# Performance work log

Hardware: AMD Instinct MI355X
Metric: run time of the kernel (lower is better)

Reference implementation:

```python
import jax, jax.numpy as jnp
import numpy as np

B, IN, HS, NM = 256, 512, 512, 1

def setup_inputs() -> dict:
    key = jax.random.key(0)
    ks = jax.random.split(key, 12)
    def kaiming(k, shape):
        fan_in = shape[0]
        bound = float(np.sqrt(6.0 / fan_in))  # kaiming_uniform with a=sqrt(5) approx; use gain sqrt(2): bound = sqrt(6/fan_in)
        return jax.random.uniform(k, shape, jnp.float32, -bound, bound)
    return {
        "x_t":  jax.random.normal(ks[0], (B, IN), jnp.float32),
        "h_t":  jax.random.normal(ks[1], (B, HS), jnp.float32),
        "c_t":  jax.random.normal(ks[2], (B, HS), jnp.float32),
        "hebb": jax.random.normal(ks[3], (B, HS, HS), jnp.float32) * 0.1,
        "W":    kaiming(ks[4], (IN, 4 * HS)),
        "U":    kaiming(ks[5], (HS, 4 * HS)),
        "bias": jnp.zeros((4 * HS,), jnp.float32),
        "alpha": jax.random.normal(ks[6], (1, 1, HS), jnp.float32) * 1e-4,
        "nm_w": jax.random.normal(ks[7], (NM, HS), jnp.float32),
        "nm_b": jnp.zeros((NM,), jnp.float32),
        "mt_w": jax.random.normal(ks[8], (HS, NM), jnp.float32),
        "mt_b": jnp.zeros((HS,), jnp.float32),
    }

def reference(x_t, h_t, c_t, hebb, W, U, bias, alpha, nm_w, nm_b, mt_w, mt_b):
    # g_t_hebb = h_t (B,1,HS) @ (alpha*hebb) (B,HS,HS) -> (B,HS)
    g_t_hebb = jnp.einsum('bh,bhk->bk', h_t, alpha * hebb)
    gates = x_t @ W + h_t @ U + bias                        # (B, 4*HS)
    i_t = jax.nn.sigmoid(gates[:, :HS])
    f_t = jax.nn.sigmoid(gates[:, HS:2 * HS])
    g_t = jnp.tanh(gates[:, 2 * HS:3 * HS] + g_t_hebb)
    o_t = jax.nn.sigmoid(gates[:, 3 * HS:])
    # rank-1 outer product per batch element: (B,HS,1)@(B,1,HS)
    delta_hebb = jnp.einsum('bi,bj->bij', h_t, g_t)         # (B,HS,HS)
    m_t = jnp.tanh(h_t @ nm_w.T + nm_b)                     # (B,NM)
    m_t = m_t @ mt_w.T + mt_b                               # (B,HS)
    hebb_new = jnp.clip(hebb + m_t[:, None, :] * delta_hebb, -2.0, 2.0)
    c_new = f_t * c_t + i_t * g_t
    h_new = o_t * jnp.tanh(c_new)
    return h_new, c_new, hebb_new
```

## Files before the change

kernel.cpp:

```cpp
#include <hip/hip_runtime.h>
#include <math.h>


#define HSZ 512
#define G4  2048

__device__ __forceinline__ float sigm(float x) { return 1.0f / (1.0f + __expf(-x)); }
__device__ __forceinline__ float clip2(float v) { return fminf(fmaxf(v, -2.0f), 2.0f); }

__global__ __launch_bounds__(256, 4)
void gates_gemm(const float* __restrict__ x, const float* __restrict__ h,
                const float* __restrict__ W, const float* __restrict__ U,
                const float* __restrict__ bias, float* __restrict__ gates)
{
    __shared__ float As[16][68];
    __shared__ float Bs[16][64];

    const int t     = threadIdx.x;
    const int brow0 = blockIdx.y * 64;
    const int bcol0 = blockIdx.x * 64;

    const int tr = t & 15;
    const int tc = t >> 4;
    const int arow = t >> 2, ak4 = (t & 3) * 4;
    const int brow = t >> 4, bc4 = (t & 15) * 4;

    float acc[4][4] = {};

    for (int ks = 0; ks < 64; ++ks) {
        const float* srcA;
        const float* srcB;
        int k0;
        if (ks < 32) { srcA = x; srcB = W; k0 = ks * 16; }
        else         { srcA = h; srcB = U; k0 = ks * 16 - 512; }

        float4 av = *(const float4*)&srcA[(size_t)(brow0 + arow) * 512 + k0 + ak4];
        float4 bv = *(const float4*)&srcB[(size_t)(k0 + brow) * 2048 + bcol0 + bc4];

        __syncthreads();
        As[ak4 + 0][arow] = av.x;
        As[ak4 + 1][arow] = av.y;
        As[ak4 + 2][arow] = av.z;
        As[ak4 + 3][arow] = av.w;
        *(float4*)&Bs[brow][bc4] = bv;
        __syncthreads();

        #pragma unroll
        for (int kk = 0; kk < 16; ++kk) {
            float4 a = *(float4*)&As[kk][tr * 4];
            float4 b = *(float4*)&Bs[kk][tc * 4];
            acc[0][0] += a.x * b.x; acc[0][1] += a.x * b.y; acc[0][2] += a.x * b.z; acc[0][3] += a.x * b.w;
            acc[1][0] += a.y * b.x; acc[1][1] += a.y * b.y; acc[1][2] += a.y * b.z; acc[1][3] += a.y * b.w;
            acc[2][0] += a.z * b.x; acc[2][1] += a.z * b.y; acc[2][2] += a.z * b.z; acc[2][3] += a.z * b.w;
            acc[3][0] += a.w * b.x; acc[3][1] += a.w * b.y; acc[3][2] += a.w * b.z; acc[3][3] += a.w * b.w;
        }
    }

    float4 bb = *(const float4*)&bias[bcol0 + tc * 4];
    #pragma unroll
    for (int rr = 0; rr < 4; ++rr) {
        const int row = brow0 + tr * 4 + rr;
        float4 o;
        o.x = acc[rr][0] + bb.x;
        o.y = acc[rr][1] + bb.y;
        o.z = acc[rr][2] + bb.z;
        o.w = acc[rr][3] + bb.w;
        *(float4*)&gates[(size_t)row * 2048 + bcol0 + tc * 4] = o;
    }
}

__global__ __launch_bounds__(256, 4)
void hebb_fused(const float* __restrict__ h_t, const float* __restrict__ c_t,
                const float* __restrict__ hebb, const float* __restrict__ alpha,
                const float* __restrict__ nm_w, const float* __restrict__ nm_b,
                const float* __restrict__ mt_w, const float* __restrict__ mt_b,
                const float* __restrict__ gates, float* __restrict__ out)
{
    const int b   = blockIdx.x >> 4;
    const int jt  = blockIdx.x & 15;
    const int j0  = jt * 32;
    const int t   = threadIdx.x;
    const int tj4 = t & 7;
    const int ti  = t >> 3;

    __shared__ float hsh[512];
    __shared__ float red[32][32];
    __shared__ float upd[32];
    __shared__ float redm[256];
    __shared__ float msh;

    const float4* hb    = (const float4*)(hebb + (size_t)b * 262144);
    const int     cbase = (j0 >> 2) + tj4;
    float4 r[16];
    #pragma unroll
    for (int k = 0; k < 16; ++k)
        r[k] = hb[(size_t)(ti * 16 + k) * 128 + cbase];

    hsh[t]       = h_t[(size_t)b * 512 + t];
    hsh[t + 256] = h_t[(size_t)b * 512 + t + 256];
    __syncthreads();

    redm[t] = hsh[t] * nm_w[t] + hsh[t + 256] * nm_w[t + 256];
    __syncthreads();
    if (t < 128) redm[t] += redm[t + 128];
    __syncthreads();
    if (t < 64)  redm[t] += redm[t + 64];
    __syncthreads();
    if (t < 64) {
        float v = redm[t];
        #pragma unroll
        for (int off = 32; off > 0; off >>= 1) v += __shfl_down(v, off);
        if (t == 0) msh = tanhf(v + nm_b[0]);
    }

    float4 ps = {0.f, 0.f, 0.f, 0.f};
    #pragma unroll
    for (int k = 0; k < 16; ++k) {
        const float hv = hsh[ti * 16 + k];
        ps.x += hv * r[k].x;
        ps.y += hv * r[k].y;
        ps.z += hv * r[k].z;
        ps.w += hv * r[k].w;
    }
    *(float4*)&red[ti][tj4 * 4] = ps;
    __syncthreads();

    if (t < 32) {
        float s = 0.f;
        #pragma unroll
        for (int q = 0; q < 32; ++q) s += red[q][t];
        const int j = j0 + t;
        const size_t gbase = (size_t)b * 2048;
        const float g  = tanhf(gates[gbase + 1024 + j] + alpha[j] * s);
        const float mm = msh * mt_w[j] + mt_b[j];
        upd[t] = mm * g;
        const float it_ = sigm(gates[gbase + j]);
        const float ft  = sigm(gates[gbase + 512 + j]);
        const float ot  = sigm(gates[gbase + 1536 + j]);
        const float cn  = ft * c_t[(size_t)b * 512 + j] + it_ * g;
        out[(size_t)b * 512 + j]          = ot * tanhf(cn);
        out[131072 + (size_t)b * 512 + j] = cn;
    }
    __syncthreads();

    const float4 u = *(float4*)&upd[tj4 * 4];
    float4* ho = (float4*)(out + 262144 + (size_t)b * 262144);
    #pragma unroll
    for (int k = 0; k < 16; ++k) {
        const float hv = hsh[ti * 16 + k];
        float4 w;
        w.x = clip2(r[k].x + u.x * hv);
        w.y = clip2(r[k].y + u.y * hv);
        w.z = clip2(r[k].z + u.z * hv);
        w.w = clip2(r[k].w + u.w * hv);
        ho[(size_t)(ti * 16 + k) * 128 + cbase] = w;
    }
}

extern "C" void kernel_launch(void* const* d_in, const int* in_sizes, int n_in,
                              void* d_out, int out_size, void* d_ws, size_t ws_size,
                              hipStream_t stream)
{
    const float* x_t   = (const float*)d_in[0];
    const float* h_t   = (const float*)d_in[1];
    const float* c_t   = (const float*)d_in[2];
    const float* hebb  = (const float*)d_in[3];
    const float* W     = (const float*)d_in[4];
    const float* U     = (const float*)d_in[5];
    const float* bias  = (const float*)d_in[6];
    const float* alpha = (const float*)d_in[7];
    const float* nm_w  = (const float*)d_in[8];
    const float* nm_b  = (const float*)d_in[9];
    const float* mt_w  = (const float*)d_in[10];
    const float* mt_b  = (const float*)d_in[11];
    float* out   = (float*)d_out;
    float* gates = (float*)d_ws;

    dim3 g1(32, 4);
    gates_gemm<<<g1, 256, 0, stream>>>(x_t, h_t, W, U, bias, gates);
    hebb_fused<<<4096, 256, 0, stream>>>(h_t, c_t, hebb, alpha, nm_w, nm_b,
                                         mt_w, mt_b, gates, out);
}
```

Before: 544.4 us.

## Retile gates GEMM to 64x32 tiles and widen hebb blocks to 512 threads

The gates GEMM moves from 64x64 output tiles with K-step 16 to 64x32 tiles with K-step 64. Each thread now computes one row by 8 columns, and the grid doubles to 256 blocks so more CUs are busy. The hebb kernel processes 64 columns per block with 512 threads, which halves the block count and simplifies the neuromodulator reduction into one pass. The hebb stream is memory-bound, so the main gains would come from GEMM occupancy and lower per-block overhead. The trade-offs are higher register pressure from 512-thread blocks and less reuse per thread in the GEMM.

```diff
diff --git a/kernel.cpp b/kernel.cpp
--- a/kernel.cpp
+++ b/kernel.cpp
@@ -1,9 +1,6 @@
 #include <hip/hip_runtime.h>
 #include <math.h>
 
-
-#define HSZ 512
-#define G4  2048
 
 __device__ __forceinline__ float sigm(float x) { return 1.0f / (1.0f + __expf(-x)); }
 __device__ __forceinline__ float clip2(float v) { return fminf(fmaxf(v, -2.0f), 2.0f); }
@@ -13,101 +10,102 @@
                 const float* __restrict__ W, const float* __restrict__ U,
                 const float* __restrict__ bias, float* __restrict__ gates)
 {
-    __shared__ float As[16][68];
-    __shared__ float Bs[16][64];
+    __shared__ float As[64][64];
+    __shared__ float Bs[64][40];
 
     const int t     = threadIdx.x;
+    const int bcol0 = blockIdx.x * 32;
     const int brow0 = blockIdx.y * 64;
-    const int bcol0 = blockIdx.x * 64;
+    const int row   = t & 63;
+    const int cg    = t >> 6;
 
-    const int tr = t & 15;
-    const int tc = t >> 4;
-    const int arow = t >> 2, ak4 = (t & 3) * 4;
-    const int brow = t >> 4, bc4 = (t & 15) * 4;
+    float acc[8] = {};
 
-    float acc[4][4] = {};
-
-    for (int ks = 0; ks < 64; ++ks) {
+    for (int ks = 0; ks < 16; ++ks) {
         const float* srcA;
         const float* srcB;
-        int k0;
-        if (ks < 32) { srcA = x; srcB = W; k0 = ks * 16; }
-        else         { srcA = h; srcB = U; k0 = ks * 16 - 512; }
+        int ka;
+        if (ks < 8) { srcA = x; srcB = W; ka = ks * 64; }
+        else        { srcA = h; srcB = U; ka = ks * 64 - 512; }
 
-        float4 av = *(const float4*)&srcA[(size_t)(brow0 + arow) * 512 + k0 + ak4];
-        float4 bv = *(const float4*)&srcB[(size_t)(k0 + brow) * 2048 + bcol0 + bc4];
+        float4 av[4];
+        #pragma unroll
+        for (int m = 0; m < 4; ++m)
+            av[m] = *(const float4*)&srcA[(size_t)(brow0 + row) * 512 + ka + cg * 16 + m * 4];
+        const int kr0 = t >> 3;
+        const int c4  = t & 7;
+        float4 bv0 = *(const float4*)&srcB[(size_t)(ka + kr0)      * 2048 + bcol0 + c4 * 4];
+        float4 bv1 = *(const float4*)&srcB[(size_t)(ka + kr0 + 32) * 2048 + bcol0 + c4 * 4];
 
         __syncthreads();
-        As[ak4 + 0][arow] = av.x;
-        As[ak4 + 1][arow] = av.y;
-        As[ak4 + 2][arow] = av.z;
-        As[ak4 + 3][arow] = av.w;
-        *(float4*)&Bs[brow][bc4] = bv;
+        #pragma unroll
+        for (int m = 0; m < 4; ++m) {
+            As[cg * 16 + m * 4 + 0][row] = av[m].x;
+            As[cg * 16 + m * 4 + 1][row] = av[m].y;
+            As[cg * 16 + m * 4 + 2][row] = av[m].z;
+            As[cg * 16 + m * 4 + 3][row] = av[m].w;
+        }
+        *(float4*)&Bs[kr0][c4 * 4]      = bv0;
+        *(float4*)&Bs[kr0 + 32][c4 * 4] = bv1;
         __syncthreads();
 
         #pragma unroll
-        for (int kk = 0; kk < 16; ++kk) {
-            float4 a = *(float4*)&As[kk][tr * 4];
-            float4 b = *(float4*)&Bs[kk][tc * 4];
-            acc[0][0] += a.x * b.x; acc[0][1] += a.x * b.y; acc[0][2] += a.x * b.z; acc[0][3] += a.x * b.w;
-            acc[1][0] += a.y * b.x; acc[1][1] += a.y * b.y; acc[1][2] += a.y * b.z; acc[1][3] += a.y * b.w;
-            acc[2][0] += a.z * b.x; acc[2][1] += a.z * b.y; acc[2][2] += a.z * b.z; acc[2][3] += a.z * b.w;
-            acc[3][0] += a.w * b.x; acc[3][1] += a.w * b.y; acc[3][2] += a.w * b.z; acc[3][3] += a.w * b.w;
+        for (int k = 0; k < 64; ++k) {
+            const float a = As[k][row];
+            const float4 b0 = *(const float4*)&Bs[k][cg * 8];
+            const float4 b1 = *(const float4*)&Bs[k][cg * 8 + 4];
+            acc[0] += a * b0.x; acc[1] += a * b0.y; acc[2] += a * b0.z; acc[3] += a * b0.w;
+            acc[4] += a * b1.x; acc[5] += a * b1.y; acc[6] += a * b1.z; acc[7] += a * b1.w;
         }
     }
 
-    float4 bb = *(const float4*)&bias[bcol0 + tc * 4];
-    #pragma unroll
-    for (int rr = 0; rr < 4; ++rr) {
-        const int row = brow0 + tr * 4 + rr;
-        float4 o;
-        o.x = acc[rr][0] + bb.x;
-        o.y = acc[rr][1] + bb.y;
-        o.z = acc[rr][2] + bb.z;
-        o.w = acc[rr][3] + bb.w;
-        *(float4*)&gates[(size_t)row * 2048 + bcol0 + tc * 4] = o;
-    }
+    const int colb = bcol0 + cg * 8;
+    float4 o0, o1;
+    o0.x = acc[0] + bias[colb + 0]; o0.y = acc[1] + bias[colb + 1];
+    o0.z = acc[2] + bias[colb + 2]; o0.w = acc[3] + bias[colb + 3];
+    o1.x = acc[4] + bias[colb + 4]; o1.y = acc[5] + bias[colb + 5];
+    o1.z = acc[6] + bias[colb + 6]; o1.w = acc[7] + bias[colb + 7];
+    float* gp = &gates[(size_t)(brow0 + row) * 2048 + colb];
+    *(float4*)gp       = o0;
+    *(float4*)(gp + 4) = o1;
 }
 
-__global__ __launch_bounds__(256, 4)
+__global__ __launch_bounds__(512, 4)
 void hebb_fused(const float* __restrict__ h_t, const float* __restrict__ c_t,
                 const float* __restrict__ hebb, const float* __restrict__ alpha,
                 const float* __restrict__ nm_w, const float* __restrict__ nm_b,
                 const float* __restrict__ mt_w, const float* __restrict__ mt_b,
                 const float* __restrict__ gates, float* __restrict__ out)
 {
-    const int b   = blockIdx.x >> 4;
-    const int jt  = blockIdx.x & 15;
-    const int j0  = jt * 32;
+    const int b   = blockIdx.x >> 3;
+    const int jt  = blockIdx.x & 7;
+    const int j0  = jt * 64;
     const int t   = threadIdx.x;
-    const int tj4 = t & 7;
-    const int ti  = t >> 3;
+    const int tj4 = t & 15;
+    const int ti  = t >> 4;
 
     __shared__ float hsh[512];
-    __shared__ float red[32][32];
-    __shared__ float upd[32];
-    __shared__ float redm[256];
+    __shared__ float red[32][64];
+    __shared__ float upd[64];
+    __shared__ float redm[512];
     __shared__ float msh;
 
     const float4* hb    = (const float4*)(hebb + (size_t)b * 262144);
-    const int     cbase = (j0 >> 2) + tj4;
+    const int     cbase = jt * 16 + tj4;
     float4 r[16];
     #pragma unroll
     for (int k = 0; k < 16; ++k)
         r[k] = hb[(size_t)(ti * 16 + k) * 128 + cbase];
 
-    hsh[t]       = h_t[(size_t)b * 512 + t];
-    hsh[t + 256] = h_t[(size_t)b * 512 + t + 256];
+    const float hv0 = h_t[(size_t)b * 512 + t];
+    hsh[t]  = hv0;
+    redm[t] = hv0 * nm_w[t];
     __syncthreads();
 
-    redm[t] = hsh[t] * nm_w[t] + hsh[t + 256] * nm_w[t + 256];
-    __syncthreads();
-    if (t < 128) redm[t] += redm[t + 128];
-    __syncthreads();
-    if (t < 64)  redm[t] += redm[t + 64];
-    __syncthreads();
     if (t < 64) {
-        float v = redm[t];
+        float v = 0.f;
+        #pragma unroll
+        for (int q = 0; q < 8; ++q) v += redm[t + q * 64];
         #pragma unroll
         for (int off = 32; off > 0; off >>= 1) v += __shfl_down(v, off);
         if (t == 0) msh = tanhf(v + nm_b[0]);
@@ -125,7 +123,7 @@
     *(float4*)&red[ti][tj4 * 4] = ps;
     __syncthreads();
 
-    if (t < 32) {
+    if (t < 64) {
         float s = 0.f;
         #pragma unroll
         for (int q = 0; q < 32; ++q) s += red[q][t];
@@ -143,7 +141,7 @@
     }
     __syncthreads();
 
-    const float4 u = *(float4*)&upd[tj4 * 4];
+    const float4 u = *(const float4*)&upd[tj4 * 4];
     float4* ho = (float4*)(out + 262144 + (size_t)b * 262144);
     #pragma unroll
     for (int k = 0; k < 16; ++k) {
@@ -176,8 +174,8 @@
     float* out   = (float*)d_out;
     float* gates = (float*)d_ws;
 
-    dim3 g1(32, 4);
+    dim3 g1(64, 4);
     gates_gemm<<<g1, 256, 0, stream>>>(x_t, h_t, W, U, bias, gates);
-    hebb_fused<<<4096, 256, 0, stream>>>(h_t, c_t, hebb, alpha, nm_w, nm_b,
+    hebb_fused<<<2048, 512, 0, stream>>>(h_t, c_t, hebb, alpha, nm_w, nm_b,
                                          mt_w, mt_b, gates, out);
 }
```

After: 505.8 us. -7.1%, faster.
